# Kernel optimization log

Measured on AMD Instinct MI355X. Metric: run time of the kernel, lower is better.

## Reference

```python
import jax, jax.numpy as jnp
import numpy as np

B, T, E, H = 128, 256, 512, 8
D = E // H  # head_dim = 64
F = 4 * E   # ffn hidden = 2048
EPS = 1e-5


def layer_norm(x, g, b):
    mu = jnp.mean(x, axis=-1, keepdims=True)
    var = jnp.mean(jnp.square(x - mu), axis=-1, keepdims=True)
    return (x - mu) * jax.lax.rsqrt(var + EPS) * g + b


def setup_inputs() -> dict:
    key = jax.random.key(0)
    ks = jax.random.split(key, 12)
    s_e = 1.0 / np.sqrt(E)
    s_f = 1.0 / np.sqrt(F)
    return {
        "x": jax.random.normal(ks[0], (B, T, E), dtype=jnp.float32),
        "Wq": jax.random.uniform(ks[1], (H, E, D), jnp.float32, -s_e, s_e),
        "Wk": jax.random.uniform(ks[2], (H, E, D), jnp.float32, -s_e, s_e),
        "Wv": jax.random.uniform(ks[3], (H, E, D), jnp.float32, -s_e, s_e),
        "Wo": jax.random.uniform(ks[4], (E, E), jnp.float32, -s_e, s_e),
        "bo": jax.random.uniform(ks[5], (E,), jnp.float32, -s_e, s_e),
        "ln1_g": jnp.ones((E,), jnp.float32),
        "ln1_b": jnp.zeros((E,), jnp.float32),
        "ln2_g": jnp.ones((E,), jnp.float32),
        "ln2_b": jnp.zeros((E,), jnp.float32),
        "W1": jax.random.uniform(ks[6], (E, F), jnp.float32, -s_e, s_e),
        "b1": jax.random.uniform(ks[7], (F,), jnp.float32, -s_e, s_e),
        "W2": jax.random.uniform(ks[8], (F, E), jnp.float32, -s_f, s_f),
        "b2": jax.random.uniform(ks[9], (E,), jnp.float32, -s_f, s_f),
    }


def reference(x, Wq, Wk, Wv, Wo, bo, ln1_g, ln1_b, ln2_g, ln2_b, W1, b1, W2, b2):
    # --- multi-head causal self-attention on ln1(x) (dropout = identity, eval mode) ---
    h = layer_norm(x, ln1_g, ln1_b)                       # [B,T,E]
    q = jnp.einsum('bte,hed->bhtd', h, Wq)
    k = jnp.einsum('bte,hed->bhtd', h, Wk)
    v = jnp.einsum('bte,hed->bhtd', h, Wv)
    scores = jnp.einsum('bhtd,bhsd->bhts', q, k) * (D ** -0.5)  # [B,H,T,T]
    causal = jnp.tril(jnp.ones((T, T), dtype=bool))
    scores = jnp.where(causal, scores, -jnp.inf)
    attn = jax.nn.softmax(scores, axis=-1)
    ctx = jnp.einsum('bhts,bhsd->bhtd', attn, v)          # [B,H,T,D]
    ctx = jnp.transpose(ctx, (0, 2, 1, 3)).reshape(B, T, E)  # concat heads
    x = ctx @ Wo + bo + x
    # --- FFN on ln2(x) ---
    h2 = layer_norm(x, ln2_g, ln2_b)
    ff = jax.nn.relu(h2 @ W1 + b1) @ W2 + b2
    return x + ff
```

## Files before the change

kernel.cpp:

```cpp
#include <hip/hip_runtime.h>


typedef unsigned short u16;
typedef short short8 __attribute__((ext_vector_type(8)));
typedef float f32x4 __attribute__((ext_vector_type(4)));

#define BB 128
#define TT 256
#define EE 512
#define HH 8
#define DD 64
#define FF 2048
#define BT (BB * TT)

__device__ __forceinline__ u16 f2b(float f) {
  union { float f; unsigned int u; } v; v.f = f;
  unsigned int u = v.u + 0x7fffu + ((v.u >> 16) & 1u);
  return (u16)(u >> 16);
}

__device__ __forceinline__ f32x4 mfma16(short8 a, short8 b, f32x4 c) {
  return __builtin_amdgcn_mfma_f32_16x16x32_bf16(a, b, c, 0, 0, 0);
}


__global__ __launch_bounds__(256) void conv_qkv(const float* __restrict__ Wq,
                                                const float* __restrict__ Wk,
                                                const float* __restrict__ Wv,
                                                u16* __restrict__ dst) {
  const int n = blockIdx.x;
  const int which = n >> 9, hd = n & 511;
  const int h = hd >> 6, d = hd & 63;
  const float* W = (which == 0) ? Wq : (which == 1) ? Wk : Wv;
  const float* src = W + (size_t)h * EE * DD + d;
  u16* drow = dst + (size_t)n * EE;
  for (int e = threadIdx.x; e < EE; e += 256)
    drow[e] = f2b(src[(size_t)e * DD]);
}

__global__ __launch_bounds__(256) void conv_t(const float* __restrict__ src,
                                              u16* __restrict__ dst, int K, int N) {
  const int n = blockIdx.x;
  u16* drow = dst + (size_t)n * K;
  for (int k = threadIdx.x; k < K; k += 256)
    drow[k] = f2b(src[(size_t)k * N + n]);
}


__global__ __launch_bounds__(256) void ln_fwd(const float* __restrict__ xin,
                                              const float* __restrict__ g,
                                              const float* __restrict__ bb,
                                              u16* __restrict__ out) {
  const int wid = threadIdx.x >> 6, lane = threadIdx.x & 63;
  const size_t row = (size_t)blockIdx.x * 4 + wid;
  const float* xr = xin + row * EE + lane * 8;
  float v[8];
  *(float4*)(v)     = *(const float4*)(xr);
  *(float4*)(v + 4) = *(const float4*)(xr + 4);
  float s = 0.f;
#pragma unroll
  for (int j = 0; j < 8; j++) s += v[j];
#pragma unroll
  for (int d = 1; d < 64; d <<= 1) s += __shfl_xor(s, d);
  const float mu = s * (1.f / 512.f);
  float q = 0.f;
#pragma unroll
  for (int j = 0; j < 8; j++) { float dd = v[j] - mu; q += dd * dd; }
#pragma unroll
  for (int d = 1; d < 64; d <<= 1) q += __shfl_xor(q, d);
  const float rstd = rsqrtf(q * (1.f / 512.f) + 1e-5f);
  float gv[8], bv[8];
  *(float4*)(gv)     = *(const float4*)(g + lane * 8);
  *(float4*)(gv + 4) = *(const float4*)(g + lane * 8 + 4);
  *(float4*)(bv)     = *(const float4*)(bb + lane * 8);
  *(float4*)(bv + 4) = *(const float4*)(bb + lane * 8 + 4);
  short8 o;
#pragma unroll
  for (int j = 0; j < 8; j++) o[j] = (short)f2b((v[j] - mu) * rstd * gv[j] + bv[j]);
  *(short8*)(out + row * EE + lane * 8) = o;
}


template <bool BIAS, bool RELU, bool RES, bool OUTBF>
__global__ __launch_bounds__(256) void gemm_bt(const u16* __restrict__ A,
                                               const u16* __restrict__ Bt,
                                               const float* __restrict__ bias,
                                               const float* __restrict__ res,
                                               void* __restrict__ out,
                                               int M, int N, int K) {
  __shared__ u16 As[128][48];
  __shared__ u16 Bs[128][48];
  const int tid = threadIdx.x;
  const int wid = tid >> 6, lane = tid & 63;
  const int llo = lane & 15, lhi = lane >> 4;
  const int wr = (wid >> 1) * 64, wc = (wid & 1) * 64;
  const size_t row0 = (size_t)blockIdx.y * 128;
  const size_t col0 = (size_t)blockIdx.x * 128;

  f32x4 acc[4][4];
#pragma unroll
  for (int m = 0; m < 4; m++)
#pragma unroll
    for (int n = 0; n < 4; n++) acc[m][n] = (f32x4){0.f, 0.f, 0.f, 0.f};

  for (int k0 = 0; k0 < K; k0 += 32) {
    __syncthreads();
#pragma unroll
    for (int p = 0; p < 2; p++) {
      const int c = p * 256 + tid;
      const int r = c >> 2, cc = (c & 3) * 8;
      *(short8*)(&As[r][cc]) = *(const short8*)(A + (row0 + r) * K + k0 + cc);
      *(short8*)(&Bs[r][cc]) = *(const short8*)(Bt + (col0 + r) * K + k0 + cc);
    }
    __syncthreads();
    short8 af[4], bf[4];
#pragma unroll
    for (int m = 0; m < 4; m++) af[m] = *(const short8*)(&As[wr + m * 16 + llo][lhi * 8]);
#pragma unroll
    for (int n = 0; n < 4; n++) bf[n] = *(const short8*)(&Bs[wc + n * 16 + llo][lhi * 8]);
#pragma unroll
    for (int m = 0; m < 4; m++)
#pragma unroll
      for (int n = 0; n < 4; n++) acc[m][n] = mfma16(af[m], bf[n], acc[m][n]);
  }

#pragma unroll
  for (int m = 0; m < 4; m++)
#pragma unroll
    for (int r = 0; r < 4; r++) {
      const size_t row = row0 + wr + m * 16 + lhi * 4 + r;
#pragma unroll
      for (int n = 0; n < 4; n++) {
        const size_t col = col0 + wc + n * 16 + llo;
        float v = acc[m][n][r];
        if (BIAS) v += bias[col];
        if (RELU) v = fmaxf(v, 0.f);
        if (RES) v += res[row * (size_t)N + col];
        if (OUTBF) ((u16*)out)[row * (size_t)N + col] = f2b(v);
        else       ((float*)out)[row * (size_t)N + col] = v;
      }
    }
}


__global__ __launch_bounds__(256) void attn_fwd(const u16* __restrict__ qkv,
                                                u16* __restrict__ ctx) {
  const int bh = blockIdx.x;
  const int b = bh >> 3, h = bh & 7;
  const int wid = threadIdx.x >> 6;
  const int lane = threadIdx.x & 63;
  const int llo = lane & 15, lhi = lane >> 4;
  const int t0 = wid * 64;

  __shared__ u16 Pl[4][64][32];

  const u16* qp = qkv + (size_t)b * TT * 1536 + h * 64;
  const u16* kp = qp + 512;
  const u16* vp = qp + 1024;

  short8 qf[4][2];
#pragma unroll
  for (int m = 0; m < 4; m++)
#pragma unroll
    for (int k2 = 0; k2 < 2; k2++) {
      const int t = t0 + m * 16 + llo;
      qf[m][k2] = *(const short8*)(qp + (size_t)t * 1536 + k2 * 32 + lhi * 8);
    }

  f32x4 O[4][4];
  float mrow[4][4], lrow[4][4];
#pragma unroll
  for (int m = 0; m < 4; m++) {
#pragma unroll
    for (int n = 0; n < 4; n++) O[m][n] = (f32x4){0.f, 0.f, 0.f, 0.f};
#pragma unroll
    for (int r = 0; r < 4; r++) { mrow[m][r] = -1e30f; lrow[m][r] = 0.f; }
  }

  const int nst = (t0 + 64) >> 5;
  for (int st = 0; st < nst; st++) {
    const int s0 = st * 32;
    f32x4 S[4][2];
#pragma unroll
    for (int m = 0; m < 4; m++) {
      S[m][0] = (f32x4){0.f, 0.f, 0.f, 0.f};
      S[m][1] = (f32x4){0.f, 0.f, 0.f, 0.f};
    }
#pragma unroll
    for (int k2 = 0; k2 < 2; k2++) {
      const short8 b0 = *(const short8*)(kp + (size_t)(s0 + llo) * 1536 + k2 * 32 + lhi * 8);
      const short8 b1 = *(const short8*)(kp + (size_t)(s0 + 16 + llo) * 1536 + k2 * 32 + lhi * 8);
#pragma unroll
      for (int m = 0; m < 4; m++) {
        S[m][0] = mfma16(qf[m][k2], b0, S[m][0]);
        S[m][1] = mfma16(qf[m][k2], b1, S[m][1]);
      }
    }
#pragma unroll
    for (int m = 0; m < 4; m++) {
      float sf[4];
#pragma unroll
      for (int r = 0; r < 4; r++) {
        const int t = t0 + m * 16 + lhi * 4 + r;
        float v0 = S[m][0][r] * 0.125f;
        float v1 = S[m][1][r] * 0.125f;
        if (s0 + llo > t)      v0 = -1e30f;
        if (s0 + 16 + llo > t) v1 = -1e30f;
        float mx = fmaxf(v0, v1);
#pragma unroll
        for (int d = 1; d < 16; d <<= 1) mx = fmaxf(mx, __shfl_xor(mx, d));
        const float mnew = fmaxf(mrow[m][r], mx);
        const float sc = __expf(mrow[m][r] - mnew);
        mrow[m][r] = mnew;
        const float p0 = __expf(v0 - mnew);
        const float p1 = __expf(v1 - mnew);
        float rs = p0 + p1;
#pragma unroll
        for (int d = 1; d < 16; d <<= 1) rs += __shfl_xor(rs, d);
        lrow[m][r] = lrow[m][r] * sc + rs;
        sf[r] = sc;
        const int pr = m * 16 + lhi * 4 + r;
        Pl[wid][pr][llo]      = f2b(p0);
        Pl[wid][pr][llo + 16] = f2b(p1);
      }
#pragma unroll
      for (int n = 0; n < 4; n++)
#pragma unroll
        for (int r = 0; r < 4; r++) O[m][n][r] *= sf[r];
    }
    short8 pf[4];
#pragma unroll
    for (int m = 0; m < 4; m++)
      pf[m] = *(const short8*)(&Pl[wid][m * 16 + llo][lhi * 8]);
#pragma unroll
    for (int n = 0; n < 4; n++) {
      short8 vf;
#pragma unroll
      for (int j = 0; j < 8; j++)
        vf[j] = (short)vp[(size_t)(s0 + lhi * 8 + j) * 1536 + n * 16 + llo];
#pragma unroll
      for (int m = 0; m < 4; m++) O[m][n] = mfma16(pf[m], vf, O[m][n]);
    }
  }

#pragma unroll
  for (int m = 0; m < 4; m++)
#pragma unroll
    for (int r = 0; r < 4; r++) {
      const int t = t0 + m * 16 + lhi * 4 + r;
      const float inv = 1.f / lrow[m][r];
      u16* orow = ctx + ((size_t)b * TT + t) * EE + h * 64;
#pragma unroll
      for (int n = 0; n < 4; n++)
        orow[n * 16 + llo] = f2b(O[m][n][r] * inv);
    }
}


extern "C" void kernel_launch(void* const* d_in, const int* in_sizes, int n_in,
                              void* d_out, int out_size, void* d_ws, size_t ws_size,
                              hipStream_t stream) {
  const float* x   = (const float*)d_in[0];
  const float* Wq  = (const float*)d_in[1];
  const float* Wk  = (const float*)d_in[2];
  const float* Wv  = (const float*)d_in[3];
  const float* Wo  = (const float*)d_in[4];
  const float* bo  = (const float*)d_in[5];
  const float* g1  = (const float*)d_in[6];
  const float* be1 = (const float*)d_in[7];
  const float* g2  = (const float*)d_in[8];
  const float* be2 = (const float*)d_in[9];
  const float* W1  = (const float*)d_in[10];
  const float* b1  = (const float*)d_in[11];
  const float* W2  = (const float*)d_in[12];
  const float* b2  = (const float*)d_in[13];
  float* out = (float*)d_out;

  char* w = (char*)d_ws;
  u16* WqkvT = (u16*)w;                 w += (size_t)1536 * 512 * 2;
  u16* WoT   = (u16*)w;                 w += (size_t)512 * 512 * 2;
  u16* W1T   = (u16*)w;                 w += (size_t)2048 * 512 * 2;
  u16* W2T   = (u16*)w;                 w += (size_t)512 * 2048 * 2;
  u16* hbuf  = (u16*)w;                 w += (size_t)BT * EE * 2;
  u16* ctxb  = (u16*)w;                 w += (size_t)BT * EE * 2;
  u16* big   = (u16*)w;
  u16* qkvb = big;
  u16* ff1  = big;

  conv_qkv<<<1536, 256, 0, stream>>>(Wq, Wk, Wv, WqkvT);
  conv_t<<<512,  256, 0, stream>>>(Wo, WoT, 512, 512);
  conv_t<<<2048, 256, 0, stream>>>(W1, W1T, 512, 2048);
  conv_t<<<512,  256, 0, stream>>>(W2, W2T, 2048, 512);

  ln_fwd<<<BT / 4, 256, 0, stream>>>(x, g1, be1, hbuf);

  gemm_bt<false, false, false, true><<<dim3(1536 / 128, BT / 128), 256, 0, stream>>>(
      hbuf, WqkvT, nullptr, nullptr, qkvb, BT, 1536, 512);

  attn_fwd<<<BB * HH, 256, 0, stream>>>(qkvb, ctxb);

  gemm_bt<true, false, true, false><<<dim3(512 / 128, BT / 128), 256, 0, stream>>>(
      ctxb, WoT, bo, x, out, BT, 512, 512);

  ln_fwd<<<BT / 4, 256, 0, stream>>>(out, g2, be2, hbuf);

  gemm_bt<true, true, false, true><<<dim3(2048 / 128, BT / 128), 256, 0, stream>>>(
      hbuf, W1T, b1, nullptr, ff1, BT, 2048, 512);

  gemm_bt<true, false, true, false><<<dim3(512 / 128, BT / 128), 256, 0, stream>>>(
      ff1, W2T, b2, out, out, BT, 512, 2048);
}
```

Measured before the change: 674.6 us.

## Tile weight transposes, use direct-to-LDS GEMM loads, swizzle blocks, stage V in LDS

The per-column weight conversion kernels become 64x64 tiled transposes through shared memory, so both reads and writes are coalesced. The GEMM now loads its A/B tiles with global_load_lds straight into unpadded shared memory and remaps block IDs in groups of eight to improve L2 locality. Attention transposes the whole V head into shared memory once per block, replacing strided scalar global gathers with vector LDS reads. The unpadded GEMM tiles may cause LDS bank conflicts on the fragment reads, and the extra V buffer raises shared-memory use per block.

After: 648.8 us. 3.8% less time.

```diff
diff --git a/kernel.cpp b/kernel.cpp
--- a/kernel.cpp
+++ b/kernel.cpp
@@ -23,27 +23,50 @@
   return __builtin_amdgcn_mfma_f32_16x16x32_bf16(a, b, c, 0, 0, 0);
 }
 
-
-__global__ __launch_bounds__(256) void conv_qkv(const float* __restrict__ Wq,
-                                                const float* __restrict__ Wk,
-                                                const float* __restrict__ Wv,
-                                                u16* __restrict__ dst) {
-  const int n = blockIdx.x;
-  const int which = n >> 9, hd = n & 511;
-  const int h = hd >> 6, d = hd & 63;
-  const float* W = (which == 0) ? Wq : (which == 1) ? Wk : Wv;
-  const float* src = W + (size_t)h * EE * DD + d;
-  u16* drow = dst + (size_t)n * EE;
-  for (int e = threadIdx.x; e < EE; e += 256)
-    drow[e] = f2b(src[(size_t)e * DD]);
-}
-
-__global__ __launch_bounds__(256) void conv_t(const float* __restrict__ src,
-                                              u16* __restrict__ dst, int K, int N) {
-  const int n = blockIdx.x;
-  u16* drow = dst + (size_t)n * K;
-  for (int k = threadIdx.x; k < K; k += 256)
-    drow[k] = f2b(src[(size_t)k * N + n]);
+__device__ __forceinline__ void g2l16(const u16* g, u16* l) {
+  __builtin_amdgcn_global_load_lds(
+      (const __attribute__((address_space(1))) unsigned int*)g,
+      (__attribute__((address_space(3))) unsigned int*)l, 16, 0, 0);
+}
+
+
+__global__ __launch_bounds__(256) void tconv(const float* __restrict__ src, int srs,
+                                             u16* __restrict__ dst, int drs) {
+  __shared__ u16 tile[64][67];
+  const int r0 = blockIdx.x * 64, c0 = blockIdx.y * 64;
+  const int tlo = threadIdx.x & 63, thi = threadIdx.x >> 6;
+#pragma unroll
+  for (int i = 0; i < 16; i++) {
+    const int r = i * 4 + thi;
+    tile[r][tlo] = f2b(src[(size_t)(r0 + r) * srs + c0 + tlo]);
+  }
+  __syncthreads();
+#pragma unroll
+  for (int i = 0; i < 16; i++) {
+    const int c = i * 4 + thi;
+    dst[(size_t)(c0 + c) * drs + r0 + tlo] = tile[tlo][c];
+  }
+}
+
+__global__ __launch_bounds__(256) void tconv_qkv(const float* __restrict__ W,
+                                                 u16* __restrict__ dst0, int nbase) {
+  __shared__ u16 tile[64][67];
+  const int h = blockIdx.z;
+  const float* src = W + (size_t)h * EE * DD;
+  u16* dst = dst0 + (size_t)(nbase + h * 64) * EE;
+  const int r0 = blockIdx.x * 64;
+  const int tlo = threadIdx.x & 63, thi = threadIdx.x >> 6;
+#pragma unroll
+  for (int i = 0; i < 16; i++) {
+    const int r = i * 4 + thi;
+    tile[r][tlo] = f2b(src[(size_t)(r0 + r) * DD + tlo]);
+  }
+  __syncthreads();
+#pragma unroll
+  for (int i = 0; i < 16; i++) {
+    const int d = i * 4 + thi;
+    dst[(size_t)d * EE + r0 + tlo] = tile[tlo][d];
+  }
 }
 
 
@@ -88,14 +111,19 @@
                                                const float* __restrict__ res,
                                                void* __restrict__ out,
                                                int M, int N, int K) {
-  __shared__ u16 As[128][48];
-  __shared__ u16 Bs[128][48];
+  __shared__ u16 As[128 * 32];
+  __shared__ u16 Bs[128 * 32];
   const int tid = threadIdx.x;
   const int wid = tid >> 6, lane = tid & 63;
   const int llo = lane & 15, lhi = lane >> 4;
   const int wr = (wid >> 1) * 64, wc = (wid & 1) * 64;
-  const size_t row0 = (size_t)blockIdx.y * 128;
-  const size_t col0 = (size_t)blockIdx.x * 128;
+
+  const int gx = gridDim.x;
+  const int nwg = gx * gridDim.y;
+  int id = blockIdx.y * gx + blockIdx.x;
+  id = (id & 7) * (nwg >> 3) + (id >> 3);
+  const size_t row0 = (size_t)(id / gx) * 128;
+  const size_t col0 = (size_t)(id % gx) * 128;
 
   f32x4 acc[4][4];
 #pragma unroll
@@ -106,18 +134,18 @@
   for (int k0 = 0; k0 < K; k0 += 32) {
     __syncthreads();
 #pragma unroll
-    for (int p = 0; p < 2; p++) {
-      const int c = p * 256 + tid;
-      const int r = c >> 2, cc = (c & 3) * 8;
-      *(short8*)(&As[r][cc]) = *(const short8*)(A + (row0 + r) * K + k0 + cc);
-      *(short8*)(&Bs[r][cc]) = *(const short8*)(Bt + (col0 + r) * K + k0 + cc);
+    for (int i = 0; i < 2; i++) {
+      const int cb = i * 256 + wid * 64;
+      const int c = cb + lane;
+      g2l16(A + (row0 + (c >> 2)) * K + k0 + (c & 3) * 8, As + cb * 8);
+      g2l16(Bt + (col0 + (c >> 2)) * K + k0 + (c & 3) * 8, Bs + cb * 8);
     }
     __syncthreads();
     short8 af[4], bf[4];
 #pragma unroll
-    for (int m = 0; m < 4; m++) af[m] = *(const short8*)(&As[wr + m * 16 + llo][lhi * 8]);
-#pragma unroll
-    for (int n = 0; n < 4; n++) bf[n] = *(const short8*)(&Bs[wc + n * 16 + llo][lhi * 8]);
+    for (int m = 0; m < 4; m++) af[m] = *(const short8*)(As + (wr + m * 16 + llo) * 32 + lhi * 8);
+#pragma unroll
+    for (int n = 0; n < 4; n++) bf[n] = *(const short8*)(Bs + (wc + n * 16 + llo) * 32 + lhi * 8);
 #pragma unroll
     for (int m = 0; m < 4; m++)
 #pragma unroll
@@ -152,12 +180,24 @@
   const int llo = lane & 15, lhi = lane >> 4;
   const int t0 = wid * 64;
 
+  __shared__ u16 Vt[64][264];
   __shared__ u16 Pl[4][64][32];
 
   const u16* qp = qkv + (size_t)b * TT * 1536 + h * 64;
   const u16* kp = qp + 512;
   const u16* vp = qp + 1024;
 
+  {
+    const int j = lane & 7;
+#pragma unroll
+    for (int g8 = 0; g8 < 8; g8++) {
+      const int s = wid * 64 + g8 * 8 + (lane >> 3);
+      const short8 v = *(const short8*)(vp + (size_t)s * 1536 + j * 8);
+#pragma unroll
+      for (int jj = 0; jj < 8; jj++) Vt[j * 8 + jj][s] = (u16)v[jj];
+    }
+  }
+
   short8 qf[4][2];
 #pragma unroll
   for (int m = 0; m < 4; m++)
@@ -176,6 +216,8 @@
 #pragma unroll
     for (int r = 0; r < 4; r++) { mrow[m][r] = -1e30f; lrow[m][r] = 0.f; }
   }
+
+  __syncthreads();
 
   const int nst = (t0 + 64) >> 5;
   for (int st = 0; st < nst; st++) {
@@ -234,10 +276,7 @@
       pf[m] = *(const short8*)(&Pl[wid][m * 16 + llo][lhi * 8]);
 #pragma unroll
     for (int n = 0; n < 4; n++) {
-      short8 vf;
-#pragma unroll
-      for (int j = 0; j < 8; j++)
-        vf[j] = (short)vp[(size_t)(s0 + lhi * 8 + j) * 1536 + n * 16 + llo];
+      const short8 vf = *(const short8*)(&Vt[n * 16 + llo][s0 + lhi * 8]);
 #pragma unroll
       for (int m = 0; m < 4; m++) O[m][n] = mfma16(pf[m], vf, O[m][n]);
     }
@@ -287,10 +326,12 @@
   u16* qkvb = big;
   u16* ff1  = big;
 
-  conv_qkv<<<1536, 256, 0, stream>>>(Wq, Wk, Wv, WqkvT);
-  conv_t<<<512,  256, 0, stream>>>(Wo, WoT, 512, 512);
-  conv_t<<<2048, 256, 0, stream>>>(W1, W1T, 512, 2048);
-  conv_t<<<512,  256, 0, stream>>>(W2, W2T, 2048, 512);
+  tconv_qkv<<<dim3(8, 1, 8), 256, 0, stream>>>(Wq, WqkvT, 0);
+  tconv_qkv<<<dim3(8, 1, 8), 256, 0, stream>>>(Wk, WqkvT, 512);
+  tconv_qkv<<<dim3(8, 1, 8), 256, 0, stream>>>(Wv, WqkvT, 1024);
+  tconv<<<dim3(8, 8),  256, 0, stream>>>(Wo, 512,  WoT, 512);
+  tconv<<<dim3(8, 32), 256, 0, stream>>>(W1, 2048, W1T, 512);
+  tconv<<<dim3(32, 8), 256, 0, stream>>>(W2, 512,  W2T, 2048);
 
   ln_fwd<<<BT / 4, 256, 0, stream>>>(x, g1, be1, hbuf);
 
```
